# Optimization experiments

Measured on AMD Instinct MI355X. Metric: run time of the kernel, lower is better.

Reference implementation:

```python
import jax, jax.numpy as jnp
import numpy as np

B, C_IN, T, N = 16, 64, 12, 1024
KS, C_OUT = 3, 64


def setup_inputs() -> dict:
    key = jax.random.key(0)
    k1, k2, k3 = jax.random.split(key, 3)
    x = jax.random.normal(k1, (B, C_IN, T, N), dtype=jnp.float32)
    # graph Chebyshev kernel [N, Ks*N]; scale down so matmuls stay well-conditioned
    kernel = jax.random.normal(k2, (N, KS * N), dtype=jnp.float32) / np.sqrt(N)
    # xavier-uniform theta [Ks*c_in, c_out]
    limit = np.sqrt(6.0 / (KS * C_IN + C_OUT))
    theta = jax.random.uniform(k3, (KS * C_IN, C_OUT), dtype=jnp.float32,
                               minval=-limit, maxval=limit)
    bias = jnp.zeros((C_OUT,), dtype=jnp.float32)
    return {"x": x, "kernel": kernel, "theta": theta, "bias": bias}


def reference(x, kernel, theta, bias):
    # x: [B, C, T, N]; kernel: [N, Ks*N] viewed as [N, Ks, N]; theta: [C*Ks, c_out]
    Bb, C, Tt, Nn = x.shape
    Ks = kernel.shape[1] // Nn
    Kr = kernel.reshape(Nn, Ks, Nn)            # [n, k, m]
    th = theta.reshape(C, Ks, -1)              # [c, k, o] (row index = c*Ks + k)
    # batched spectral conv over all timesteps at once (fuses the per-t loop)
    x_mul = jnp.einsum('bctn,nkm->bctkm', x, Kr)       # [B,C,T,Ks,N]
    gc = jnp.einsum('bctkm,cko->botm', x_mul, th)      # [B,c_out,T,N]
    gc = gc + bias[None, :, None, None]
    # c_in == c_out -> residual is identity
    return jax.nn.relu(gc + x)
```

## Files before the change

kernel.cpp:

```cpp
#include <hip/hip_runtime.h>

#define NB   16
#define NC   64
#define NT   12
#define NN   1024
#define NKS  3

typedef float  f32x4  __attribute__((ext_vector_type(4)));
typedef short  s16x8  __attribute__((ext_vector_type(8)));
typedef unsigned short u16x4 __attribute__((ext_vector_type(4)));
typedef unsigned short u16x8 __attribute__((ext_vector_type(8)));

__device__ __forceinline__ unsigned short f2bf(float f) {
    union { float f; unsigned u; } v; v.f = f;
    unsigned r = v.u + 0x7FFFu + ((v.u >> 16) & 1u);
    return (unsigned short)(r >> 16);
}

__device__ __forceinline__ void cp16(const void* g, void* l) {
    __builtin_amdgcn_global_load_lds(
        (const __attribute__((address_space(1))) unsigned int*)g,
        (__attribute__((address_space(3))) unsigned int*)l, 16, 0, 0);
}

#define APAN_OFF 0
#define KB_OFF   25165824
#define TH_OFF   31457280

__global__ __launch_bounds__(256)
void spatio_prep(const float* __restrict__ x, const float* __restrict__ kern,
                 const float* __restrict__ theta,
                 unsigned short* __restrict__ apan, unsigned short* __restrict__ kb,
                 unsigned short* __restrict__ thbf)
{
    const int blk = blockIdx.x;
    const int tid = threadIdx.x;

    if (blk < 6144) {
        int id   = blk * 256 + tid;
        int slot = id & 1023;
        int g4nb = id >> 10;
        int nb   = g4nb & 31, g4 = g4nb >> 5;
        int row  = slot >> 2, p = slot & 3;
        int d    = p ^ (row & 3);
        int bl   = row >> 6, c = row & 63;
        int bt   = 4 * g4 + bl;
        int b    = bt / NT, t = bt - NT * b;
        const float* src = x + ((size_t)((b * NC + c) * NT + t)) * NN + nb * 32 + d * 8;
        float4 a0 = ((const float4*)src)[0];
        float4 a1 = ((const float4*)src)[1];
        u16x8 w;
        w[0] = f2bf(a0.x); w[1] = f2bf(a0.y); w[2] = f2bf(a0.z); w[3] = f2bf(a0.w);
        w[4] = f2bf(a1.x); w[5] = f2bf(a1.y); w[6] = f2bf(a1.z); w[7] = f2bf(a1.w);
        ((u16x8*)apan)[id] = w;
    } else if (blk < 6528) {
        int id   = (blk - 6144) * 256 + tid;
        int j    = id % 192;
        int rest = id / 192;
        int nb   = rest & 31, mt = rest >> 5;
        int k    = j >> 6, mm = j & 63;
        int col  = (k << 10) + (mt << 6) + mm;
        size_t base = ((size_t)(mt * 32 + nb) * 768) + j * 4;
#pragma unroll
        for (int d = 0; d < 4; ++d) {
            u16x8 w;
#pragma unroll
            for (int i = 0; i < 8; ++i) {
                int n = nb * 32 + d * 8 + i;
                w[i] = f2bf(kern[(size_t)n * (NKS * NN) + col]);
            }
            ((u16x8*)kb)[base + (d ^ (j & 3))] = w;
        }
    } else {
        int id = (blk - 6528) * 256 + tid;
        if (id < 12288) {
            int row = id >> 6, o = id & 63;
            int c = row / 3, k = row - 3 * c;
            thbf[o * 192 + k * 64 + c] = f2bf(theta[id]);
        }
    }
}

__global__ __launch_bounds__(256, 2)
void spatio_main(const unsigned short* __restrict__ apan,
                 const unsigned short* __restrict__ kb,
                 const unsigned short* __restrict__ thbf,
                 const float* __restrict__ x, const float* __restrict__ bias,
                 float* __restrict__ out)
{
    __shared__ __attribute__((aligned(128))) char smem[51200];
    unsigned short (*As)[32]  = (unsigned short (*)[32])smem;
    unsigned short (*Bs)[32]  = (unsigned short (*)[32])(smem + 16384);
    unsigned short (*xm0)[200] = (unsigned short (*)[200])smem;
    unsigned short (*xm1)[200] = (unsigned short (*)[200])(smem + 25600);

    const int tid  = threadIdx.x;
    const int g4   = blockIdx.x;
    const int mt   = blockIdx.y;
    const int m_base = mt * 64;
    const int lane = tid & 63;
    const int wid  = tid >> 6;
    const int wr   = wid & 1;
    const int wn   = wid >> 1;
    const int quad = lane >> 4;
    const int l16  = lane & 15;
    const int pofs = (quad ^ (l16 & 3)) * 8;

    const char* apan_c = (const char*)apan + ((size_t)g4 << 19);
    const char* kb_c   = (const char*)kb + ((size_t)mt * 32 * 768 * 16);

    f32x4 acc[8][6];
#pragma unroll
    for (int i = 0; i < 8; ++i)
#pragma unroll
        for (int j = 0; j < 6; ++j) acc[i][j] = (f32x4){0.f, 0.f, 0.f, 0.f};

    for (int it = 0; it < 32; ++it) {
        __syncthreads();
        {
            const char* asrc = apan_c + ((size_t)it << 14);
            const char* bsrc = kb_c + ((size_t)it * 12288);
#pragma unroll
            for (int i = 0; i < 4; ++i)
                cp16(asrc + (i * 256 + tid) * 16, smem + (i * 256 + tid) * 16);
#pragma unroll
            for (int i = 0; i < 3; ++i)
                cp16(bsrc + (i * 256 + tid) * 16, smem + 16384 + (i * 256 + tid) * 16);
        }
        __syncthreads();

        s16x8 af[8], bf[6];
#pragma unroll
        for (int rb = 0; rb < 8; ++rb)
            af[rb] = *(const s16x8*)&As[128 * wr + 16 * rb + l16][pofs];
#pragma unroll
        for (int jb = 0; jb < 6; ++jb)
            bf[jb] = *(const s16x8*)&Bs[96 * wn + 16 * jb + l16][pofs];
#pragma unroll
        for (int rb = 0; rb < 8; ++rb)
#pragma unroll
            for (int jb = 0; jb < 6; ++jb)
                acc[rb][jb] = __builtin_amdgcn_mfma_f32_16x16x32_bf16(af[rb], bf[jb], acc[rb][jb], 0, 0, 0);
    }

    for (int pass = 0; pass < 2; ++pass) {
        __syncthreads();
        if (wr == pass) {
#pragma unroll
            for (int rb = 0; rb < 8; ++rb) {
                unsigned short (*dst)[200] = (rb < 4) ? xm0 : xm1;
                int ck0 = 16 * (rb & 3) + 4 * quad;
#pragma unroll
                for (int jb = 0; jb < 6; ++jb) {
                    int J  = 96 * wn + 16 * jb + l16;
                    int kk = J >> 6, mm = J & 63;
                    u16x4 w;
                    w.x = f2bf(acc[rb][jb].x); w.y = f2bf(acc[rb][jb].y);
                    w.z = f2bf(acc[rb][jb].z); w.w = f2bf(acc[rb][jb].w);
                    *(u16x4*)&dst[mm][kk * 64 + ck0] = w;
                }
            }
        }
        __syncthreads();

        const int sel = wid & 1;
        const int oh  = wid >> 1;
        unsigned short (*srcT)[200] = sel ? xm1 : xm0;

        f32x4 acc2[2][4];
#pragma unroll
        for (int ob = 0; ob < 2; ++ob)
#pragma unroll
            for (int j = 0; j < 4; ++j) acc2[ob][j] = (f32x4){0.f, 0.f, 0.f, 0.f};

#pragma unroll
        for (int ks = 0; ks < 6; ++ks) {
            s16x8 a2[2];
#pragma unroll
            for (int ob = 0; ob < 2; ++ob)
                a2[ob] = *(const s16x8*)(thbf + (size_t)(32 * oh + 16 * ob + l16) * 192 + ks * 32 + quad * 8);
#pragma unroll
            for (int jb = 0; jb < 4; ++jb) {
                s16x8 b2 = *(const s16x8*)&srcT[16 * jb + l16][ks * 32 + quad * 8];
#pragma unroll
                for (int ob = 0; ob < 2; ++ob)
                    acc2[ob][jb] = __builtin_amdgcn_mfma_f32_16x16x32_bf16(a2[ob], b2, acc2[ob][jb], 0, 0, 0);
            }
        }

        const int bt = 4 * g4 + 2 * pass + sel;
        const int b2 = bt / NT, t2 = bt - NT * b2;
#pragma unroll
        for (int ob = 0; ob < 2; ++ob)
#pragma unroll
            for (int jb = 0; jb < 4; ++jb) {
                int mm = 16 * jb + l16;
#pragma unroll
                for (int r = 0; r < 4; ++r) {
                    int o = 32 * oh + 16 * ob + 4 * quad + r;
                    size_t idx = (((size_t)(b2 * NC + o) * NT + t2) * NN) + m_base + mm;
                    float v = acc2[ob][jb][r] + bias[o] + x[idx];
                    out[idx] = fmaxf(v, 0.f);
                }
            }
    }
}

extern "C" void kernel_launch(void* const* d_in, const int* in_sizes, int n_in,
                              void* d_out, int out_size, void* d_ws, size_t ws_size,
                              hipStream_t stream) {
    const float* x     = (const float*)d_in[0];
    const float* kern  = (const float*)d_in[1];
    const float* theta = (const float*)d_in[2];
    const float* bias  = (const float*)d_in[3];
    float* out = (float*)d_out;
    (void)in_sizes; (void)n_in; (void)out_size; (void)ws_size;

    unsigned short* apan = (unsigned short*)((char*)d_ws + APAN_OFF);
    unsigned short* kbp  = (unsigned short*)((char*)d_ws + KB_OFF);
    unsigned short* thbf = (unsigned short*)((char*)d_ws + TH_OFF);

    hipLaunchKernelGGL(spatio_prep, dim3(6576), dim3(256), 0, stream,
                       x, kern, theta, apan, kbp, thbf);
    hipLaunchKernelGGL(spatio_main, dim3(48, 16), dim3(256), 0, stream,
                       apan, kbp, thbf, x, bias, out);
}
```

Measured before the change: 228.1 us.

## Halve main-kernel row tile and take residual from staged bf16 tiles

```diff
diff --git a/kernel.cpp b/kernel.cpp
--- a/kernel.cpp
+++ b/kernel.cpp
@@ -10,11 +10,16 @@
 typedef short  s16x8  __attribute__((ext_vector_type(8)));
 typedef unsigned short u16x4 __attribute__((ext_vector_type(4)));
 typedef unsigned short u16x8 __attribute__((ext_vector_type(8)));
-
-__device__ __forceinline__ unsigned short f2bf(float f) {
+typedef unsigned short ush;
+
+__device__ __forceinline__ ush f2bf(float f) {
     union { float f; unsigned u; } v; v.f = f;
     unsigned r = v.u + 0x7FFFu + ((v.u >> 16) & 1u);
-    return (unsigned short)(r >> 16);
+    return (ush)(r >> 16);
+}
+__device__ __forceinline__ float bf2f(ush h) {
+    union { unsigned u; float f; } v; v.u = ((unsigned)h) << 16;
+    return v.f;
 }
 
 __device__ __forceinline__ void cp16(const void* g, void* l) {
@@ -30,21 +35,44 @@
 __global__ __launch_bounds__(256)
 void spatio_prep(const float* __restrict__ x, const float* __restrict__ kern,
                  const float* __restrict__ theta,
-                 unsigned short* __restrict__ apan, unsigned short* __restrict__ kb,
-                 unsigned short* __restrict__ thbf)
+                 ush* __restrict__ apan, ush* __restrict__ kb, ush* __restrict__ thbf)
 {
     const int blk = blockIdx.x;
     const int tid = threadIdx.x;
 
-    if (blk < 6144) {
-        int id   = blk * 256 + tid;
-        int slot = id & 1023;
-        int g4nb = id >> 10;
-        int nb   = g4nb & 31, g4 = g4nb >> 5;
+    if (blk < 1536) {
+        int ch   = blk * 256 + tid;
+        int j    = ch % 192;
+        int rest = ch / 192;
+        int d    = rest & 3;
+        int nb   = (rest >> 2) & 31;
+        int mt   = rest >> 7;
+        int k    = j >> 6, mm = j & 63;
+        int col  = (k << 10) + (mt << 6) + mm;
+        u16x8 w;
+#pragma unroll
+        for (int i = 0; i < 8; ++i) {
+            int n = nb * 32 + d * 8 + i;
+            w[i] = f2bf(kern[(size_t)n * (NKS * NN) + col]);
+        }
+        size_t base = ((size_t)(mt * 32 + nb) * 768) + j * 4 + (d ^ (j & 3));
+        ((u16x8*)kb)[base] = w;
+    } else if (blk < 1584) {
+        int id = (blk - 1536) * 256 + tid;
+        if (id < 12288) {
+            int row = id >> 6, o = id & 63;
+            int c = row / 3, k = row - 3 * c;
+            thbf[o * 192 + k * 64 + c] = f2bf(theta[id]);
+        }
+    } else {
+        int id   = (blk - 1584) * 256 + tid;
+        int slot = id & 511;
+        int g2nb = id >> 9;
+        int nb   = g2nb & 31, g2 = g2nb >> 5;
         int row  = slot >> 2, p = slot & 3;
         int d    = p ^ (row & 3);
         int bl   = row >> 6, c = row & 63;
-        int bt   = 4 * g4 + bl;
+        int bt   = 2 * g2 + bl;
         int b    = bt / NT, t = bt - NT * b;
         const float* src = x + ((size_t)((b * NC + c) * NT + t)) * NN + nb * 32 + d * 8;
         float4 a0 = ((const float4*)src)[0];
@@ -53,49 +81,23 @@
         w[0] = f2bf(a0.x); w[1] = f2bf(a0.y); w[2] = f2bf(a0.z); w[3] = f2bf(a0.w);
         w[4] = f2bf(a1.x); w[5] = f2bf(a1.y); w[6] = f2bf(a1.z); w[7] = f2bf(a1.w);
         ((u16x8*)apan)[id] = w;
-    } else if (blk < 6528) {
-        int id   = (blk - 6144) * 256 + tid;
-        int j    = id % 192;
-        int rest = id / 192;
-        int nb   = rest & 31, mt = rest >> 5;
-        int k    = j >> 6, mm = j & 63;
-        int col  = (k << 10) + (mt << 6) + mm;
-        size_t base = ((size_t)(mt * 32 + nb) * 768) + j * 4;
-#pragma unroll
-        for (int d = 0; d < 4; ++d) {
-            u16x8 w;
-#pragma unroll
-            for (int i = 0; i < 8; ++i) {
-                int n = nb * 32 + d * 8 + i;
-                w[i] = f2bf(kern[(size_t)n * (NKS * NN) + col]);
-            }
-            ((u16x8*)kb)[base + (d ^ (j & 3))] = w;
-        }
-    } else {
-        int id = (blk - 6528) * 256 + tid;
-        if (id < 12288) {
-            int row = id >> 6, o = id & 63;
-            int c = row / 3, k = row - 3 * c;
-            thbf[o * 192 + k * 64 + c] = f2bf(theta[id]);
-        }
     }
 }
 
 __global__ __launch_bounds__(256, 2)
-void spatio_main(const unsigned short* __restrict__ apan,
-                 const unsigned short* __restrict__ kb,
-                 const unsigned short* __restrict__ thbf,
-                 const float* __restrict__ x, const float* __restrict__ bias,
+void spatio_main(const ush* __restrict__ apan, const ush* __restrict__ kb,
+                 const ush* __restrict__ thbf, const float* __restrict__ bias,
                  float* __restrict__ out)
 {
-    __shared__ __attribute__((aligned(128))) char smem[51200];
-    unsigned short (*As)[32]  = (unsigned short (*)[32])smem;
-    unsigned short (*Bs)[32]  = (unsigned short (*)[32])(smem + 16384);
-    unsigned short (*xm0)[200] = (unsigned short (*)[200])smem;
-    unsigned short (*xm1)[200] = (unsigned short (*)[200])(smem + 25600);
+    __shared__ __attribute__((aligned(128))) char smem[41984];
+    ush (*As)[32]  = (ush (*)[32])smem;
+    ush (*Bs)[32]  = (ush (*)[32])(smem + 8192);
+    ush (*xm)[200] = (ush (*)[200])smem;
+    ush (*stL)[32] = (ush (*)[32])(smem + 25600);
+    ush (*stH)[32] = (ush (*)[32])(smem + 33792);
 
     const int tid  = threadIdx.x;
-    const int g4   = blockIdx.x;
+    const int g2   = blockIdx.x;
     const int mt   = blockIdx.y;
     const int m_base = mt * 64;
     const int lane = tid & 63;
@@ -106,103 +108,100 @@
     const int l16  = lane & 15;
     const int pofs = (quad ^ (l16 & 3)) * 8;
 
-    const char* apan_c = (const char*)apan + ((size_t)g4 << 19);
+    const char* apan_c = (const char*)apan + ((size_t)g2 << 18);
     const char* kb_c   = (const char*)kb + ((size_t)mt * 32 * 768 * 16);
 
-    f32x4 acc[8][6];
-#pragma unroll
-    for (int i = 0; i < 8; ++i)
+    f32x4 acc[4][6];
+#pragma unroll
+    for (int i = 0; i < 4; ++i)
 #pragma unroll
         for (int j = 0; j < 6; ++j) acc[i][j] = (f32x4){0.f, 0.f, 0.f, 0.f};
 
     for (int it = 0; it < 32; ++it) {
         __syncthreads();
-        {
-            const char* asrc = apan_c + ((size_t)it << 14);
-            const char* bsrc = kb_c + ((size_t)it * 12288);
-#pragma unroll
-            for (int i = 0; i < 4; ++i)
-                cp16(asrc + (i * 256 + tid) * 16, smem + (i * 256 + tid) * 16);
-#pragma unroll
-            for (int i = 0; i < 3; ++i)
-                cp16(bsrc + (i * 256 + tid) * 16, smem + 16384 + (i * 256 + tid) * 16);
-        }
-        __syncthreads();
-
-        s16x8 af[8], bf[6];
-#pragma unroll
-        for (int rb = 0; rb < 8; ++rb)
-            af[rb] = *(const s16x8*)&As[128 * wr + 16 * rb + l16][pofs];
+        const char* asrc = apan_c + ((size_t)it << 13);
+        const char* bsrc = kb_c + ((size_t)it * 12288);
+#pragma unroll
+        for (int i = 0; i < 2; ++i)
+            cp16(asrc + (i * 256 + tid) * 16, smem + (i * 256 + tid) * 16);
+#pragma unroll
+        for (int i = 0; i < 3; ++i)
+            cp16(bsrc + (i * 256 + tid) * 16, smem + 8192 + (i * 256 + tid) * 16);
+        if ((it >> 1) == mt) {
+            char* sb = smem + 25600 + (it & 1) * 8192;
+#pragma unroll
+            for (int i = 0; i < 2; ++i) {
+                int m = i * 256 + tid;
+                int slot = (m & ~3) + ((m & 3) ^ ((m >> 2) & 3));
+                cp16(asrc + slot * 16, sb + m * 16);
+            }
+        }
+        __syncthreads();
+
+        s16x8 af[4], bf[6];
+#pragma unroll
+        for (int rb = 0; rb < 4; ++rb)
+            af[rb] = *(const s16x8*)&As[64 * wr + 16 * rb + l16][pofs];
 #pragma unroll
         for (int jb = 0; jb < 6; ++jb)
             bf[jb] = *(const s16x8*)&Bs[96 * wn + 16 * jb + l16][pofs];
 #pragma unroll
-        for (int rb = 0; rb < 8; ++rb)
+        for (int rb = 0; rb < 4; ++rb)
 #pragma unroll
             for (int jb = 0; jb < 6; ++jb)
                 acc[rb][jb] = __builtin_amdgcn_mfma_f32_16x16x32_bf16(af[rb], bf[jb], acc[rb][jb], 0, 0, 0);
     }
 
+    float bo[4];
+#pragma unroll
+    for (int r = 0; r < 4; ++r) bo[r] = bias[16 * wid + 4 * quad + r];
+
     for (int pass = 0; pass < 2; ++pass) {
         __syncthreads();
         if (wr == pass) {
 #pragma unroll
-            for (int rb = 0; rb < 8; ++rb) {
-                unsigned short (*dst)[200] = (rb < 4) ? xm0 : xm1;
-                int ck0 = 16 * (rb & 3) + 4 * quad;
+            for (int rb = 0; rb < 4; ++rb)
 #pragma unroll
                 for (int jb = 0; jb < 6; ++jb) {
                     int J  = 96 * wn + 16 * jb + l16;
                     int kk = J >> 6, mm = J & 63;
+                    int ck0 = kk * 64 + 16 * rb + 4 * quad;
                     u16x4 w;
                     w.x = f2bf(acc[rb][jb].x); w.y = f2bf(acc[rb][jb].y);
                     w.z = f2bf(acc[rb][jb].z); w.w = f2bf(acc[rb][jb].w);
-                    *(u16x4*)&dst[mm][kk * 64 + ck0] = w;
+                    *(u16x4*)&xm[mm][ck0] = w;
                 }
+        }
+        __syncthreads();
+
+        f32x4 acc2[4];
+#pragma unroll
+        for (int jb = 0; jb < 4; ++jb) acc2[jb] = (f32x4){0.f, 0.f, 0.f, 0.f};
+#pragma unroll
+        for (int ks = 0; ks < 6; ++ks) {
+            s16x8 a2 = *(const s16x8*)(thbf + (size_t)(16 * wid + l16) * 192 + ks * 32 + quad * 8);
+#pragma unroll
+            for (int jb = 0; jb < 4; ++jb) {
+                s16x8 b2 = *(const s16x8*)&xm[16 * jb + l16][ks * 32 + quad * 8];
+                acc2[jb] = __builtin_amdgcn_mfma_f32_16x16x32_bf16(a2, b2, acc2[jb], 0, 0, 0);
             }
         }
-        __syncthreads();
-
-        const int sel = wid & 1;
-        const int oh  = wid >> 1;
-        unsigned short (*srcT)[200] = sel ? xm1 : xm0;
-
-        f32x4 acc2[2][4];
-#pragma unroll
-        for (int ob = 0; ob < 2; ++ob)
-#pragma unroll
-            for (int j = 0; j < 4; ++j) acc2[ob][j] = (f32x4){0.f, 0.f, 0.f, 0.f};
-
-#pragma unroll
-        for (int ks = 0; ks < 6; ++ks) {
-            s16x8 a2[2];
-#pragma unroll
-            for (int ob = 0; ob < 2; ++ob)
-                a2[ob] = *(const s16x8*)(thbf + (size_t)(32 * oh + 16 * ob + l16) * 192 + ks * 32 + quad * 8);
-#pragma unroll
-            for (int jb = 0; jb < 4; ++jb) {
-                s16x8 b2 = *(const s16x8*)&srcT[16 * jb + l16][ks * 32 + quad * 8];
-#pragma unroll
-                for (int ob = 0; ob < 2; ++ob)
-                    acc2[ob][jb] = __builtin_amdgcn_mfma_f32_16x16x32_bf16(a2[ob], b2, acc2[ob][jb], 0, 0, 0);
+
+        const int bt = 2 * g2 + pass;
+        const int b2i = bt / NT, t2 = bt - NT * b2i;
+#pragma unroll
+        for (int jb = 0; jb < 4; ++jb) {
+            int mm = 16 * jb + l16;
+#pragma unroll
+            for (int r = 0; r < 4; ++r) {
+                int o = 16 * wid + 4 * quad + r;
+                int row = pass * 64 + o;
+                ush rv = (jb < 2) ? stL[row][mm] : stH[row][mm - 32];
+                size_t idx = (((size_t)(b2i * NC + o) * NT + t2) * NN) + m_base + mm;
+                float v = acc2[jb][r] + bo[r] + bf2f(rv);
+                out[idx] = fmaxf(v, 0.f);
             }
         }
-
-        const int bt = 4 * g4 + 2 * pass + sel;
-        const int b2 = bt / NT, t2 = bt - NT * b2;
-#pragma unroll
-        for (int ob = 0; ob < 2; ++ob)
-#pragma unroll
-            for (int jb = 0; jb < 4; ++jb) {
-                int mm = 16 * jb + l16;
-#pragma unroll
-                for (int r = 0; r < 4; ++r) {
-                    int o = 32 * oh + 16 * ob + 4 * quad + r;
-                    size_t idx = (((size_t)(b2 * NC + o) * NT + t2) * NN) + m_base + mm;
-                    float v = acc2[ob][jb][r] + bias[o] + x[idx];
-                    out[idx] = fmaxf(v, 0.f);
-                }
-            }
     }
 }
 
@@ -216,12 +215,12 @@
     float* out = (float*)d_out;
     (void)in_sizes; (void)n_in; (void)out_size; (void)ws_size;
 
-    unsigned short* apan = (unsigned short*)((char*)d_ws + APAN_OFF);
-    unsigned short* kbp  = (unsigned short*)((char*)d_ws + KB_OFF);
-    unsigned short* thbf = (unsigned short*)((char*)d_ws + TH_OFF);
-
-    hipLaunchKernelGGL(spatio_prep, dim3(6576), dim3(256), 0, stream,
+    ush* apan = (ush*)((char*)d_ws + APAN_OFF);
+    ush* kbp  = (ush*)((char*)d_ws + KB_OFF);
+    ush* thbf = (ush*)((char*)d_ws + TH_OFF);
+
+    hipLaunchKernelGGL(spatio_prep, dim3(7728), dim3(256), 0, stream,
                        x, kern, theta, apan, kbp, thbf);
-    hipLaunchKernelGGL(spatio_main, dim3(48, 16), dim3(256), 0, stream,
-                       apan, kbp, thbf, x, bias, out);
-}
+    hipLaunchKernelGGL(spatio_main, dim3(96, 16), dim3(256), 0, stream,
+                       apan, kbp, thbf, bias, out);
+}
```

Result: faster. 188.6 us (-17.3%).
